# Optimization experiments

Hardware: AMD Instinct MI355X
Metric: run time of the kernel (lower is better)

## Reference

```python
import jax, jax.numpy as jnp
import numpy as np

N = 100000
E = 1600000
IN_DIM = 256
HID = 128


def gcn_conv(x, edge_index, W, b):
    # x: [N, F_in], edge_index: [2, E] (row=source, col=target)
    h = x @ W  # [N, F_out]
    n = x.shape[0]
    loops = jnp.arange(n, dtype=edge_index.dtype)
    row = jnp.concatenate([edge_index[0], loops])
    col = jnp.concatenate([edge_index[1], loops])
    w = jnp.ones(row.shape[0], dtype=h.dtype)
    deg = jax.ops.segment_sum(w, col, num_segments=n)
    dinv = jnp.where(deg > 0, jax.lax.rsqrt(deg), 0.0)
    norm = dinv[row] * dinv[col]  # [E+N]
    msgs = h[row] * norm[:, None]  # gather + scale
    out = jax.ops.segment_sum(msgs, col, num_segments=n)  # scatter-add at targets
    return out + b


def setup_inputs() -> dict:
    key = jax.random.key(0)
    ks = jax.random.split(key, 8)
    x = jax.random.normal(ks[0], (N, IN_DIM), dtype=jnp.float32)
    edge_index = jax.random.randint(ks[1], (2, E), 0, N, dtype=jnp.int64)
    s1 = 1.0 / np.sqrt(IN_DIM)
    s2 = 1.0 / np.sqrt(HID)
    W1 = jax.random.uniform(ks[2], (IN_DIM, HID), jnp.float32, -s1, s1)
    b1 = jnp.zeros((HID,), jnp.float32)
    W2 = jax.random.uniform(ks[3], (HID, HID), jnp.float32, -s2, s2)
    b2 = jnp.zeros((HID,), jnp.float32)
    Wp = jax.random.uniform(ks[4], (HID, HID), jnp.float32, -s2, s2)
    bp = jax.random.uniform(ks[5], (HID,), jnp.float32, -s2, s2)
    return {"x": x, "edge_index": edge_index, "W1": W1, "b1": b1,
            "W2": W2, "b2": b2, "Wp": Wp, "bp": bp}


def reference(x, edge_index, W1, b1, W2, b2, Wp, bp):
    # Faithful GConv.forward with conv='gcn': two GCNConv layers (no
    # activation/dropout/norm applied in the original forward), then a
    # linear projection head; returns (z, projection(z)).
    z = gcn_conv(x, edge_index, W1, b1)
    z = gcn_conv(z, edge_index, W2, b2)
    proj = z @ Wp + bp
    return (z, proj)
```

## Files before the change

### kernel.cpp

```cpp
#include <hip/hip_runtime.h>

typedef __attribute__((ext_vector_type(8))) short short8;
typedef __attribute__((ext_vector_type(4))) float f32x4;

__device__ __forceinline__ float bf2f(unsigned short u) {
    union { unsigned int i; float f; } v; v.i = ((unsigned int)u) << 16; return v.f;
}
__device__ __forceinline__ unsigned short f2bf(float f) {
    union { float f; unsigned int i; } v; v.f = f;
    unsigned int i = v.i;
    return (unsigned short)((i + 0x7FFFu + ((i >> 16) & 1u)) >> 16);
}
__device__ __forceinline__ float ldext(const void* p, size_t i, int xf) {
    return xf ? ((const float*)p)[i] : bf2f(((const unsigned short*)p)[i]);
}
__device__ __forceinline__ float scrub(float v) {
    return (__builtin_fabsf(v) < 1e30f) ? v : 9.0f;
}

__global__ void k_detect(const int* __restrict__ ei, const unsigned short* __restrict__ xs,
                         int* __restrict__ flags) {
    int lane = threadIdx.x;
    int orv = 0;
    for (int i = 2 * lane + 1; i < 256; i += 128) orv |= ei[i];
    int cnt = 0;
    for (int i = lane; i < 256; i += 64) {
        int e = (xs[i] >> 7) & 0xFF;
        cnt += (e >= 97 && e <= 159) ? 1 : 0;
    }
    for (int off = 32; off > 0; off >>= 1) {
        orv |= __shfl_down(orv, off);
        cnt += __shfl_down(cnt, off);
    }
    if (lane == 0) {
        flags[0] = (orv == 0) ? 1 : 0;
        flags[1] = (cnt >= 240) ? 0 : 1;
    }
}

#define BSH 10
#define BNODES (1 << BSH)
#define RBITS (32 - BSH)
#define EPB 16

__global__ void k_zero(int* __restrict__ p, int n) {
    int i = blockIdx.x * 256 + threadIdx.x;
    if (i < n) p[i] = 0;
}

__global__ __launch_bounds__(256) void k_bcount(const int* __restrict__ ei,
                                                const int* __restrict__ flags,
                                                int* __restrict__ bcnt,
                                                int e, int n, int nb) {
    __shared__ int hist[1024];
    int tid = threadIdx.x;
    for (int i = tid; i < 1024; i += 256) hist[i] = 0;
    __syncthreads();
    int f = flags[0];
    long base = (long)blockIdx.x * (256 * EPB);
#pragma unroll
    for (int j = 0; j < EPB; ++j) {
        long i = base + j * 256 + tid;
        if (i < e) {
            int c = ei[(e + i) << f];
            if ((unsigned)c >= (unsigned)n) c = 0;
            atomicAdd(&hist[c >> BSH], 1);
        }
    }
    __syncthreads();
    for (int b = tid; b < nb; b += 256) {
        int h = hist[b];
        if (h) atomicAdd(&bcnt[b], h);
    }
}

__global__ __launch_bounds__(1024) void k_bscan(const int* __restrict__ bcnt,
                                                int* __restrict__ boff,
                                                int* __restrict__ bcur,
                                                int nb, int e,
                                                int* __restrict__ rowptr, int n) {
    __shared__ int ws[16];
    int t = threadIdx.x, lane = t & 63, wv = t >> 6;
    int v = (t < nb) ? bcnt[t] : 0;
    int s = v;
    for (int off = 1; off < 64; off <<= 1) {
        int x = __shfl_up(s, off);
        if (lane >= off) s += x;
    }
    if (lane == 63) ws[wv] = s;
    __syncthreads();
    if (wv == 0 && lane < 16) {
        int w = ws[lane];
        for (int off = 1; off < 16; off <<= 1) {
            int x = __shfl_up(w, off);
            if (lane >= off) w += x;
        }
        ws[lane] = w;
    }
    __syncthreads();
    int excl = (wv ? ws[wv - 1] : 0) + s - v;
    if (t < nb) { boff[t] = excl; bcur[t] = excl; }
    if (t == 0) { boff[nb] = e; rowptr[n] = e; }
}

__global__ __launch_bounds__(256) void k_bin(const int* __restrict__ ei,
                                             const int* __restrict__ flags,
                                             int* __restrict__ bcur,
                                             int* __restrict__ binned,
                                             int e, int n, int nb) {
    __shared__ int hist[1024];
    __shared__ int wbase[1024];
    int tid = threadIdx.x;
    for (int i = tid; i < 1024; i += 256) hist[i] = 0;
    __syncthreads();
    int f = flags[0];
    long base = (long)blockIdx.x * (256 * EPB);
    int cs[EPB], rr[EPB];
#pragma unroll
    for (int j = 0; j < EPB; ++j) {
        long i = base + j * 256 + tid;
        int c = -1, r = 0;
        if (i < e) {
            c = ei[(e + i) << f];
            r = ei[i << f];
            if ((unsigned)c >= (unsigned)n) c = 0;
            if ((unsigned)r >= (unsigned)n) r = 0;
            atomicAdd(&hist[c >> BSH], 1);
        }
        cs[j] = c;
        rr[j] = r;
    }
    __syncthreads();
    for (int b = tid; b < nb; b += 256) {
        int h = hist[b];
        wbase[b] = h ? atomicAdd(&bcur[b], h) : 0;
    }
    __syncthreads();
    for (int i = tid; i < 1024; i += 256) hist[i] = 0;
    __syncthreads();
#pragma unroll
    for (int j = 0; j < EPB; ++j) {
        int c = cs[j];
        if (c >= 0) {
            int b = c >> BSH;
            int off = atomicAdd(&hist[b], 1);
            int rec = rr[j] | ((c & (BNODES - 1)) << RBITS);
            binned[wbase[b] + off] = rec;
        }
    }
}

__global__ __launch_bounds__(256) void k_build(const int* __restrict__ binned,
                                               const int* __restrict__ boff,
                                               int* __restrict__ rowptr,
                                               float* __restrict__ dinv,
                                               int* __restrict__ csr_src,
                                               int n) {
    __shared__ int hist[1024];
    __shared__ int ws4[4];
    int b = blockIdx.x;
    int tid = threadIdx.x;
    int v0 = b << BSH;
    int rs = boff[b], re = boff[b + 1];
    for (int i = tid; i < 1024; i += 256) hist[i] = 0;
    __syncthreads();
    for (int i = rs + tid; i < re; i += 256)
        atomicAdd(&hist[((unsigned)binned[i]) >> RBITS], 1);
    __syncthreads();
    int idx = tid * 4;
    int h0 = hist[idx], h1 = hist[idx + 1], h2 = hist[idx + 2], h3 = hist[idx + 3];
    int ls = h0 + h1 + h2 + h3;
    int lane = tid & 63, wv = tid >> 6;
    int s = ls;
    for (int off = 1; off < 64; off <<= 1) {
        int x = __shfl_up(s, off);
        if (lane >= off) s += x;
    }
    if (lane == 63) ws4[wv] = s;
    __syncthreads();
    int wb = 0;
    for (int k = 0; k < 4; ++k) wb += (k < wv) ? ws4[k] : 0;
    int excl = wb + (s - ls);
    int e0 = excl, e1 = excl + h0, e2 = e1 + h1, e3 = e2 + h2;
    hist[idx] = rs + e0; hist[idx + 1] = rs + e1;
    hist[idx + 2] = rs + e2; hist[idx + 3] = rs + e3;
    int vv = v0 + idx;
    if (vv < n)     { rowptr[vv]     = rs + e0; dinv[vv]     = rsqrtf((float)(h0 + 1)); }
    if (vv + 1 < n) { rowptr[vv + 1] = rs + e1; dinv[vv + 1] = rsqrtf((float)(h1 + 1)); }
    if (vv + 2 < n) { rowptr[vv + 2] = rs + e2; dinv[vv + 2] = rsqrtf((float)(h2 + 1)); }
    if (vv + 3 < n) { rowptr[vv + 3] = rs + e3; dinv[vv + 3] = rsqrtf((float)(h3 + 1)); }
    __syncthreads();
    for (int i = rs + tid; i < re; i += 256) {
        int rec = binned[i];
        int cl = ((unsigned)rec) >> RBITS;
        int r = rec & ((1 << RBITS) - 1);
        int pos = atomicAdd(&hist[cl], 1);
        csr_src[pos] = r;
    }
}


#define KPAD 136

__device__ __forceinline__ short8 load_frag(const void* A, size_t row, int K, int off, int f32m) {
    if (!f32m)
        return *(const short8*)((const unsigned short*)A + row * (size_t)K + off);
    const float* p = (const float*)A + row * (size_t)K + off;
    short8 r;
#pragma unroll
    for (int j = 0; j < 8; ++j) r[j] = (short)f2bf(p[j]);
    return r;
}

__global__ __launch_bounds__(256) void k_gemm(
    const void* __restrict__ A, const void* __restrict__ W,
    void* __restrict__ Cbase, const void* __restrict__ bias,
    int M, int K, const int* __restrict__ flags,
    int a_ext, int c_half, int c_ext) {
    __shared__ unsigned short lds[128 * KPAD];
    int xf = flags[1];
    int af = a_ext & xf;
    int cf = c_ext & xf;
    char* cp = (char*)Cbase + (size_t)c_half * (size_t)M * 128 * (xf ? 4 : 2);

    int tid = threadIdx.x;
    int wave = tid >> 6, lane = tid & 63;
    int quad = lane >> 4, l16 = lane & 15;
    int row0 = blockIdx.x * 128 + wave * 32;

    f32x4 acc[2][8];
    for (int m = 0; m < 2; ++m)
        for (int t = 0; t < 8; ++t)
            acc[m][t] = (f32x4){0.f, 0.f, 0.f, 0.f};

    size_t ar0 = (size_t)min(row0 + l16, M - 1);
    size_t ar1 = (size_t)min(row0 + 16 + l16, M - 1);

    for (int kc = 0; kc < K; kc += 128) {
        __syncthreads();
        if (xf) {
            for (int i = tid; i < 128 * 128; i += 256) {
                int k = i >> 7, n = i & 127;
                lds[n * KPAD + k] = f2bf(((const float*)W)[(size_t)(kc + k) * 128 + n]);
            }
        } else {
            for (int i = tid; i < 128 * 128; i += 256) {
                int k = i >> 7, n = i & 127;
                lds[n * KPAD + k] = ((const unsigned short*)W)[(size_t)(kc + k) * 128 + n];
            }
        }
        __syncthreads();
        for (int ks = 0; ks < 128; ks += 32) {
            short8 a0 = load_frag(A, ar0, K, kc + ks + quad * 8, af);
            short8 a1 = load_frag(A, ar1, K, kc + ks + quad * 8, af);
            for (int t = 0; t < 8; ++t) {
                short8 bf = *(const short8*)(&lds[(t * 16 + l16) * KPAD + ks + quad * 8]);
                acc[0][t] = __builtin_amdgcn_mfma_f32_16x16x32_bf16(a0, bf, acc[0][t], 0, 0, 0);
                acc[1][t] = __builtin_amdgcn_mfma_f32_16x16x32_bf16(a1, bf, acc[1][t], 0, 0, 0);
            }
        }
    }
    for (int t = 0; t < 8; ++t) {
        int colx = t * 16 + l16;
        float bv = bias ? ldext(bias, colx, xf) : 0.f;
        for (int m = 0; m < 2; ++m) {
            for (int r = 0; r < 4; ++r) {
                int row = row0 + m * 16 + quad * 4 + r;
                if (row < M) {
                    float v = scrub(acc[m][t][r] + bv);
                    if (cf) ((float*)cp)[(size_t)row * 128 + colx] = v;
                    else ((unsigned short*)cp)[(size_t)row * 128 + colx] = f2bf(v);
                }
            }
        }
    }
}


__global__ __launch_bounds__(256) void k_agg(
    const void* __restrict__ hbase, int h_half,
    const int* __restrict__ rowptr, const int* __restrict__ csr_src,
    const float* __restrict__ dinv, const void* __restrict__ bias,
    void* __restrict__ z, int z_ext,
    int n, int etot, const int* __restrict__ flags) {
    int v = (blockIdx.x * 256 + threadIdx.x) >> 4;
    if (v >= n) return;
    int xf = flags[1];
    int zf = z_ext & xf;
    const unsigned short* h = (const unsigned short*)
        ((const char*)hbase + (size_t)h_half * (size_t)n * 128 * (xf ? 4 : 2));
    int g = threadIdx.x & 15;
    float di = dinv[v];
    int s = rowptr[v], e = rowptr[v + 1];
    if (e > etot) e = etot;
    if (s < 0) s = 0;

    short8 hv = *(const short8*)(h + (size_t)v * 128 + g * 8);
    float sw = di * di;
    float acc[8];
#pragma unroll
    for (int j = 0; j < 8; ++j) acc[j] = bf2f((unsigned short)hv[j]) * sw;

    int u0 = (s < e) ? csr_src[s] : 0;
    if ((unsigned)u0 >= (unsigned)n) u0 = 0;
    float du0 = dinv[u0];
    short8 h0 = *(const short8*)(h + (size_t)u0 * 128 + g * 8);
    for (int i = s; i < e; ++i) {
        int u1 = (i + 1 < e) ? csr_src[i + 1] : 0;
        if ((unsigned)u1 >= (unsigned)n) u1 = 0;
        float du1 = dinv[u1];
        short8 h1 = *(const short8*)(h + (size_t)u1 * 128 + g * 8);
        float w = di * du0;
#pragma unroll
        for (int j = 0; j < 8; ++j) acc[j] += bf2f((unsigned short)h0[j]) * w;
        u0 = u1; du0 = du1; h0 = h1;
    }

#pragma unroll
    for (int j = 0; j < 8; ++j)
        acc[j] = scrub(acc[j] + ldext(bias, g * 8 + j, xf));

    if (zf) {
        float* zp = (float*)z + (size_t)v * 128 + g * 8;
        f32x4 o0 = {acc[0], acc[1], acc[2], acc[3]};
        f32x4 o1 = {acc[4], acc[5], acc[6], acc[7]};
        *(f32x4*)zp = o0;
        *(f32x4*)(zp + 4) = o1;
    } else {
        short8 o;
#pragma unroll
        for (int j = 0; j < 8; ++j) o[j] = (short)f2bf(acc[j]);
        *(short8*)((unsigned short*)z + (size_t)v * 128 + g * 8) = o;
    }
}


static inline size_t alignup(size_t x) { return (x + 255) & ~(size_t)255; }

extern "C" void kernel_launch(void* const* d_in, const int* in_sizes, int n_in,
                              void* d_out, int out_size, void* d_ws, size_t ws_size,
                              hipStream_t stream) {
    const void* x  = d_in[0];
    const int*  ei = (const int*)d_in[1];
    const void* W1 = d_in[2];
    const void* b1 = d_in[3];
    const void* W2 = d_in[4];
    const void* b2 = d_in[5];
    const void* Wp = d_in[6];
    const void* bp = d_in[7];

    const int HID = in_sizes[3];
    const int IN_DIM = in_sizes[2] / HID;
    const int N = in_sizes[0] / IN_DIM;
    const int E = in_sizes[1] / 2;

    char* w = (char*)d_ws;
    int* flags = (int*)w;      w += 256;
    int* rowptr = (int*)w;     w += alignup(sizeof(int) * (size_t)(N + 1));
    float* dinv = (float*)w;   w += alignup(sizeof(float) * (size_t)N);
    int* bcnt = (int*)w;       w += 4096;
    int* boff = (int*)w;       w += 8192;
    int* bcur = (int*)w;       w += 4096;
    int* csr_src = (int*)w;    w += alignup(sizeof(int) * (size_t)E);
    size_t fixed = (size_t)(w - (char*)d_ws);
    size_t bufbytes = alignup((size_t)N * HID * 2);
    bool wsmode = ws_size >= fixed + 2 * bufbytes;

    int* binned = (int*)d_out;

    void* hC;  int h_half;
    void* z1p;
    if (wsmode) {
        hC = (void*)w;  h_half = 0;
        z1p = (void*)(w + bufbytes);
    } else {
        hC = d_out;     h_half = 1;
        z1p = d_out;
    }

    int nb = (N + BNODES - 1) >> BSH;
    int ebb = (E + 256 * EPB - 1) / (256 * EPB);
    int gemm_blocks = (N + 127) / 128;
    int agg_blocks = (N + 15) / 16;

    k_detect<<<1, 64, 0, stream>>>(ei, (const unsigned short*)x, flags);
    k_zero<<<(nb + 255) / 256, 256, 0, stream>>>(bcnt, nb);
    k_bcount<<<ebb, 256, 0, stream>>>(ei, flags, bcnt, E, N, nb);
    k_bscan<<<1, 1024, 0, stream>>>(bcnt, boff, bcur, nb, E, rowptr, N);
    k_bin<<<ebb, 256, 0, stream>>>(ei, flags, bcur, binned, E, N, nb);
    k_build<<<nb, 256, 0, stream>>>(binned, boff, rowptr, dinv, csr_src, N);

    k_gemm<<<gemm_blocks, 256, 0, stream>>>(x, W1, hC, nullptr, N, IN_DIM, flags,
                                            1, h_half, 0);
    k_agg<<<agg_blocks, 256, 0, stream>>>(hC, h_half, rowptr, csr_src, dinv, b1,
                                          z1p, 0, N, E, flags);

    k_gemm<<<gemm_blocks, 256, 0, stream>>>(z1p, W2, hC, nullptr, N, HID, flags,
                                            0, h_half, 0);
    k_agg<<<agg_blocks, 256, 0, stream>>>(hC, h_half, rowptr, csr_src, dinv, b2,
                                          d_out, 1, N, E, flags);

    k_gemm<<<gemm_blocks, 256, 0, stream>>>(d_out, Wp, d_out, bp, N, HID, flags,
                                            1, 1, 1);
}
```

Measured before the change: 549.1 us.

## Stage A tiles through LDS with coalesced loads and fragment-ordered W

The GEMM kernel now loads the A tile cooperatively into shared memory with wide coalesced vector loads, converting fp32 to bf16 once per element, rather than each lane gathering 8 strided elements per fragment from global memory. W is staged in LDS already arranged in MFMA fragment order, so each lane reads one short8 without bank conflicts. The K chunk shrinks from 128 to 64 to fit both tiles. The aim is better global coalescing on A. The cost is one more barrier-separated staging step per K chunk, plus strided scalar global reads of W.

```diff
diff --git a/kernel.cpp b/kernel.cpp
--- a/kernel.cpp
+++ b/kernel.cpp
@@ -200,24 +200,15 @@
 }
 
 
-#define KPAD 136
-
-__device__ __forceinline__ short8 load_frag(const void* A, size_t row, int K, int off, int f32m) {
-    if (!f32m)
-        return *(const short8*)((const unsigned short*)A + row * (size_t)K + off);
-    const float* p = (const float*)A + row * (size_t)K + off;
-    short8 r;
-#pragma unroll
-    for (int j = 0; j < 8; ++j) r[j] = (short)f2bf(p[j]);
-    return r;
-}
+#define ASTR 72
 
 __global__ __launch_bounds__(256) void k_gemm(
     const void* __restrict__ A, const void* __restrict__ W,
     void* __restrict__ Cbase, const void* __restrict__ bias,
     int M, int K, const int* __restrict__ flags,
     int a_ext, int c_half, int c_ext) {
-    __shared__ unsigned short lds[128 * KPAD];
+    __shared__ unsigned short lds_a[128 * ASTR];
+    __shared__ short8 lds_w[16 * 64];
     int xf = flags[1];
     int af = a_ext & xf;
     int cf = c_ext & xf;
@@ -226,46 +217,86 @@
     int tid = threadIdx.x;
     int wave = tid >> 6, lane = tid & 63;
     int quad = lane >> 4, l16 = lane & 15;
-    int row0 = blockIdx.x * 128 + wave * 32;
+    int row0 = blockIdx.x * 128;
 
     f32x4 acc[2][8];
     for (int m = 0; m < 2; ++m)
         for (int t = 0; t < 8; ++t)
             acc[m][t] = (f32x4){0.f, 0.f, 0.f, 0.f};
 
-    size_t ar0 = (size_t)min(row0 + l16, M - 1);
-    size_t ar1 = (size_t)min(row0 + 16 + l16, M - 1);
-
-    for (int kc = 0; kc < K; kc += 128) {
+    for (int kc = 0; kc < K; kc += 64) {
         __syncthreads();
-        if (xf) {
-            for (int i = tid; i < 128 * 128; i += 256) {
-                int k = i >> 7, n = i & 127;
-                lds[n * KPAD + k] = f2bf(((const float*)W)[(size_t)(kc + k) * 128 + n]);
+        if (af) {
+            int r = tid >> 2;
+            int kq = (tid & 3) << 4;
+#pragma unroll
+            for (int rb = 0; rb < 128; rb += 64) {
+                size_t grow = (size_t)min(row0 + rb + r, M - 1);
+                const f32x4* p = (const f32x4*)((const float*)A + grow * (size_t)K + kc + kq);
+                f32x4 v0 = p[0], v1 = p[1], v2 = p[2], v3 = p[3];
+                short8 o0, o1;
+#pragma unroll
+                for (int j = 0; j < 4; ++j) {
+                    o0[j] = (short)f2bf(v0[j]);
+                    o0[j + 4] = (short)f2bf(v1[j]);
+                    o1[j] = (short)f2bf(v2[j]);
+                    o1[j + 4] = (short)f2bf(v3[j]);
+                }
+                unsigned short* dst = &lds_a[(rb + r) * ASTR + kq];
+                *(short8*)dst = o0;
+                *(short8*)(dst + 8) = o1;
             }
         } else {
-            for (int i = tid; i < 128 * 128; i += 256) {
-                int k = i >> 7, n = i & 127;
-                lds[n * KPAD + k] = ((const unsigned short*)W)[(size_t)(kc + k) * 128 + n];
+            int r = tid >> 1;
+            int kq = (tid & 1) << 5;
+            size_t grow = (size_t)min(row0 + r, M - 1);
+            const short8* p = (const short8*)((const unsigned short*)A + grow * (size_t)K + kc + kq);
+            short8 s0 = p[0], s1 = p[1], s2 = p[2], s3 = p[3];
+            unsigned short* dst = &lds_a[r * ASTR + kq];
+            *(short8*)dst = s0;
+            *(short8*)(dst + 8) = s1;
+            *(short8*)(dst + 16) = s2;
+            *(short8*)(dst + 24) = s3;
+        }
+#pragma unroll
+        for (int p = 0; p < 4; ++p) {
+            int f = tid + p * 256;
+            int lf = f & 63, frow = f >> 6;
+            int col = ((frow & 7) << 4) + (lf & 15);
+            int k0 = kc + ((frow >> 3) << 5) + ((lf >> 4) << 3);
+            short8 val;
+            if (xf) {
+                const float* wp = (const float*)W + (size_t)k0 * 128 + col;
+#pragma unroll
+                for (int j = 0; j < 8; ++j) val[j] = (short)f2bf(wp[(size_t)j * 128]);
+            } else {
+                const unsigned short* wp = (const unsigned short*)W + (size_t)k0 * 128 + col;
+#pragma unroll
+                for (int j = 0; j < 8; ++j) val[j] = (short)wp[(size_t)j * 128];
             }
+            lds_w[f] = val;
         }
         __syncthreads();
-        for (int ks = 0; ks < 128; ks += 32) {
-            short8 a0 = load_frag(A, ar0, K, kc + ks + quad * 8, af);
-            short8 a1 = load_frag(A, ar1, K, kc + ks + quad * 8, af);
+#pragma unroll
+        for (int ks = 0; ks < 64; ks += 32) {
+            int ksg = ks >> 5;
+            short8 a0 = *(const short8*)&lds_a[(wave * 32 + l16) * ASTR + ks + quad * 8];
+            short8 a1 = *(const short8*)&lds_a[(wave * 32 + 16 + l16) * ASTR + ks + quad * 8];
+#pragma unroll
             for (int t = 0; t < 8; ++t) {
-                short8 bf = *(const short8*)(&lds[(t * 16 + l16) * KPAD + ks + quad * 8]);
+                short8 bf = lds_w[(ksg * 8 + t) * 64 + lane];
                 acc[0][t] = __builtin_amdgcn_mfma_f32_16x16x32_bf16(a0, bf, acc[0][t], 0, 0, 0);
                 acc[1][t] = __builtin_amdgcn_mfma_f32_16x16x32_bf16(a1, bf, acc[1][t], 0, 0, 0);
             }
         }
     }
+    int wrow0 = row0 + wave * 32;
     for (int t = 0; t < 8; ++t) {
         int colx = t * 16 + l16;
         float bv = bias ? ldext(bias, colx, xf) : 0.f;
         for (int m = 0; m < 2; ++m) {
             for (int r = 0; r < 4; ++r) {
-                int row = row0 + m * 16 + quad * 4 + r;
+                int row = wrow0 + m * 16 + quad * 4 + r;
                 if (row < M) {
                     float v = scrub(acc[m][t][r] + bv);
                     if (cf) ((float*)cp)[(size_t)row * 128 + colx] = v;
```

After: 543.8 us. About the same (-1.0%).

## Pre-swizzle weights into MFMA fragment layout and drop LDS staging in GEMM

Applied to the files above, without the earlier changes.

Adds a small prep kernel that converts each weight matrix once into bf16 short8 fragments laid out per lane for the MFMA B operand. The GEMM then reads B fragments straight from global memory (L2-resident) instead of having every block transpose and convert the whole weight tile into LDS behind two barriers. This removes the per-block LDS fill and its syncthreads, and waves now exit early past M. The cost is three extra tiny launches, extra workspace, and B loads that go through the cache rather than LDS on every k-step.

```diff
diff --git a/kernel.cpp b/kernel.cpp
--- a/kernel.cpp
+++ b/kernel.cpp
@@ -200,7 +200,29 @@
 }
 
 
-#define KPAD 136
+__global__ __launch_bounds__(256) void k_wprep(const void* __restrict__ W,
+                                               short8* __restrict__ Wf,
+                                               int K, const int* __restrict__ flags) {
+    int idx = blockIdx.x * 256 + threadIdx.x;
+    int total = (K >> 5) * 8 * 64;
+    if (idx >= total) return;
+    int lane = idx & 63, frow = idx >> 6;
+    int t = frow & 7, ksg = frow >> 3;
+    int col = t * 16 + (lane & 15);
+    int k0 = ksg * 32 + ((lane >> 4) << 3);
+    int xf = flags[1];
+    short8 val;
+    if (xf) {
+        const float* wp = (const float*)W + (size_t)k0 * 128 + col;
+#pragma unroll
+        for (int j = 0; j < 8; ++j) val[j] = (short)f2bf(wp[(size_t)j * 128]);
+    } else {
+        const unsigned short* wp = (const unsigned short*)W + (size_t)k0 * 128 + col;
+#pragma unroll
+        for (int j = 0; j < 8; ++j) val[j] = (short)wp[(size_t)j * 128];
+    }
+    Wf[idx] = val;
+}
 
 __device__ __forceinline__ short8 load_frag(const void* A, size_t row, int K, int off, int f32m) {
     if (!f32m)
@@ -213,11 +235,10 @@
 }
 
 __global__ __launch_bounds__(256) void k_gemm(
-    const void* __restrict__ A, const void* __restrict__ W,
+    const void* __restrict__ A, const short8* __restrict__ Wf,
     void* __restrict__ Cbase, const void* __restrict__ bias,
     int M, int K, const int* __restrict__ flags,
     int a_ext, int c_half, int c_ext) {
-    __shared__ unsigned short lds[128 * KPAD];
     int xf = flags[1];
     int af = a_ext & xf;
     int cf = c_ext & xf;
@@ -226,44 +247,40 @@
     int tid = threadIdx.x;
     int wave = tid >> 6, lane = tid & 63;
     int quad = lane >> 4, l16 = lane & 15;
-    int row0 = blockIdx.x * 128 + wave * 32;
+    int row0 = (blockIdx.x * 4 + wave) * 32;
+    if (row0 >= M) return;
 
     f32x4 acc[2][8];
+#pragma unroll
     for (int m = 0; m < 2; ++m)
+#pragma unroll
         for (int t = 0; t < 8; ++t)
             acc[m][t] = (f32x4){0.f, 0.f, 0.f, 0.f};
 
     size_t ar0 = (size_t)min(row0 + l16, M - 1);
     size_t ar1 = (size_t)min(row0 + 16 + l16, M - 1);
 
-    for (int kc = 0; kc < K; kc += 128) {
-        __syncthreads();
-        if (xf) {
-            for (int i = tid; i < 128 * 128; i += 256) {
-                int k = i >> 7, n = i & 127;
-                lds[n * KPAD + k] = f2bf(((const float*)W)[(size_t)(kc + k) * 128 + n]);
-            }
-        } else {
-            for (int i = tid; i < 128 * 128; i += 256) {
-                int k = i >> 7, n = i & 127;
-                lds[n * KPAD + k] = ((const unsigned short*)W)[(size_t)(kc + k) * 128 + n];
-            }
-        }
-        __syncthreads();
-        for (int ks = 0; ks < 128; ks += 32) {
-            short8 a0 = load_frag(A, ar0, K, kc + ks + quad * 8, af);
-            short8 a1 = load_frag(A, ar1, K, kc + ks + quad * 8, af);
-            for (int t = 0; t < 8; ++t) {
-                short8 bf = *(const short8*)(&lds[(t * 16 + l16) * KPAD + ks + quad * 8]);
-                acc[0][t] = __builtin_amdgcn_mfma_f32_16x16x32_bf16(a0, bf, acc[0][t], 0, 0, 0);
-                acc[1][t] = __builtin_amdgcn_mfma_f32_16x16x32_bf16(a1, bf, acc[1][t], 0, 0, 0);
-            }
-        }
-    }
+    int nks = K >> 5;
+#pragma unroll 2
+    for (int ksg = 0; ksg < nks; ++ksg) {
+        int k0 = (ksg << 5) + quad * 8;
+        short8 a0 = load_frag(A, ar0, K, k0, af);
+        short8 a1 = load_frag(A, ar1, K, k0, af);
+        const short8* wrow = Wf + (size_t)(ksg << 3) * 64 + lane;
+#pragma unroll
+        for (int t = 0; t < 8; ++t) {
+            short8 bf = wrow[t * 64];
+            acc[0][t] = __builtin_amdgcn_mfma_f32_16x16x32_bf16(a0, bf, acc[0][t], 0, 0, 0);
+            acc[1][t] = __builtin_amdgcn_mfma_f32_16x16x32_bf16(a1, bf, acc[1][t], 0, 0, 0);
+        }
+    }
+#pragma unroll
     for (int t = 0; t < 8; ++t) {
         int colx = t * 16 + l16;
         float bv = bias ? ldext(bias, colx, xf) : 0.f;
+#pragma unroll
         for (int m = 0; m < 2; ++m) {
+#pragma unroll
             for (int r = 0; r < 4; ++r) {
                 int row = row0 + m * 16 + quad * 4 + r;
                 if (row < M) {
@@ -361,6 +378,9 @@
     int* bcnt = (int*)w;       w += 4096;
     int* boff = (int*)w;       w += 8192;
     int* bcur = (int*)w;       w += 4096;
+    short8* wf1 = (short8*)w;  w += alignup((size_t)IN_DIM * HID * 2);
+    short8* wf2 = (short8*)w;  w += alignup((size_t)HID * HID * 2);
+    short8* wfp = (short8*)w;  w += alignup((size_t)HID * HID * 2);
     int* csr_src = (int*)w;    w += alignup(sizeof(int) * (size_t)E);
     size_t fixed = (size_t)(w - (char*)d_ws);
     size_t bufbytes = alignup((size_t)N * HID * 2);
@@ -380,26 +400,30 @@
 
     int nb = (N + BNODES - 1) >> BSH;
     int ebb = (E + 256 * EPB - 1) / (256 * EPB);
-    int gemm_blocks = (N + 127) / 128;
+    int tiles = (N + 31) / 32;
+    int gemm_blocks = (tiles + 3) / 4;
     int agg_blocks = (N + 15) / 16;
 
     k_detect<<<1, 64, 0, stream>>>(ei, (const unsigned short*)x, flags);
+    k_wprep<<<(IN_DIM * 16 + 255) / 256, 256, 0, stream>>>(W1, wf1, IN_DIM, flags);
+    k_wprep<<<(HID * 16 + 255) / 256, 256, 0, stream>>>(W2, wf2, HID, flags);
+    k_wprep<<<(HID * 16 + 255) / 256, 256, 0, stream>>>(Wp, wfp, HID, flags);
     k_zero<<<(nb + 255) / 256, 256, 0, stream>>>(bcnt, nb);
     k_bcount<<<ebb, 256, 0, stream>>>(ei, flags, bcnt, E, N, nb);
     k_bscan<<<1, 1024, 0, stream>>>(bcnt, boff, bcur, nb, E, rowptr, N);
     k_bin<<<ebb, 256, 0, stream>>>(ei, flags, bcur, binned, E, N, nb);
     k_build<<<nb, 256, 0, stream>>>(binned, boff, rowptr, dinv, csr_src, N);
 
-    k_gemm<<<gemm_blocks, 256, 0, stream>>>(x, W1, hC, nullptr, N, IN_DIM, flags,
+    k_gemm<<<gemm_blocks, 256, 0, stream>>>(x, wf1, hC, nullptr, N, IN_DIM, flags,
                                             1, h_half, 0);
     k_agg<<<agg_blocks, 256, 0, stream>>>(hC, h_half, rowptr, csr_src, dinv, b1,
                                           z1p, 0, N, E, flags);
 
-    k_gemm<<<gemm_blocks, 256, 0, stream>>>(z1p, W2, hC, nullptr, N, HID, flags,
+    k_gemm<<<gemm_blocks, 256, 0, stream>>>(z1p, wf2, hC, nullptr, N, HID, flags,
                                             0, h_half, 0);
     k_agg<<<agg_blocks, 256, 0, stream>>>(hC, h_half, rowptr, csr_src, dinv, b2,
                                           d_out, 1, N, E, flags);
 
-    k_gemm<<<gemm_blocks, 256, 0, stream>>>(d_out, Wp, d_out, bp, N, HID, flags,
+    k_gemm<<<gemm_blocks, 256, 0, stream>>>(d_out, wfp, d_out, bp, N, HID, flags,
                                             1, 1, 1);
 }
```

Result: slower. 567.4 us (+3.3%).
